# Kernel tuning notes

Measured on AMD Instinct MI355X. Metric: run time of the kernel, lower is better.

Reference implementation:

```python
import jax, jax.numpy as jnp
import numpy as np

B, N, C, H = 64, 500, 128, 256
EPS = 1e-5


def _bn(x, g, b):
    # BatchNorm1d in training mode: biased batch statistics
    m = jnp.mean(x, axis=0)
    v = jnp.mean((x - m) ** 2, axis=0)
    return g * (x - m) * jax.lax.rsqrt(v + EPS) + b


def _lin(x, w, b):
    return x @ w.T + b


def setup_inputs() -> dict:
    key = jax.random.key(0)
    ks = jax.random.split(key, 16)

    def w(k, shape, s=0.05):
        return (s * jax.random.normal(k, shape)).astype(jnp.float32)

    return {
        'l2_xyz': jax.random.uniform(ks[0], (B, 3, N), dtype=jnp.float32),
        'l2_points': jax.random.normal(ks[1], (B, C, N), dtype=jnp.float32),
        'l3_points': jax.random.normal(ks[2], (B, C), dtype=jnp.float32),
        'temp': jax.random.uniform(ks[3], (B, 1, N), dtype=jnp.float32) * 400.0,
        'fc_res0_w': w(ks[4], (H, H)), 'fc_res0_b': jnp.zeros((H,), jnp.float32),
        'bn_res0_g': jnp.ones((H,), jnp.float32), 'bn_res0_b': jnp.zeros((H,), jnp.float32),
        'fc_res1_w': w(ks[5], (H, H)), 'fc_res1_b': jnp.zeros((H,), jnp.float32),
        'bn_res1_g': jnp.ones((H,), jnp.float32), 'bn_res1_b': jnp.zeros((H,), jnp.float32),
        'fc_res2_w': w(ks[6], (H, H)), 'fc_res2_b': jnp.zeros((H,), jnp.float32),
        'bn_res2_g': jnp.ones((H,), jnp.float32), 'bn_res2_b': jnp.zeros((H,), jnp.float32),
        'fc_lt1_w': w(ks[7], (H, H)), 'fc_lt1_b': jnp.zeros((H,), jnp.float32),
        'bn_lt1_g': jnp.ones((H,), jnp.float32), 'bn_lt1_b': jnp.zeros((H,), jnp.float32),
        'fc_lt4_w': w(ks[8], (1, H)), 'fc_lt4_b': jnp.zeros((1,), jnp.float32),
    }


def reference(l2_xyz, l2_points, l3_points, temp,
              fc_res0_w, fc_res0_b, bn_res0_g, bn_res0_b,
              fc_res1_w, fc_res1_b, bn_res1_g, bn_res1_b,
              fc_res2_w, fc_res2_b, bn_res2_g, bn_res2_b,
              fc_lt1_w, fc_lt1_b, bn_lt1_g, bn_lt1_b,
              fc_lt4_w, fc_lt4_b):
    point = jnp.transpose(l2_xyz, (0, 2, 1))    # [B,N,3]
    data = jnp.transpose(l2_points, (0, 2, 1))  # [B,N,C]

    # square_distance(point, point), then abs + sqrt
    s = jnp.sum(point * point, axis=-1)  # [B,N]
    sq = s[:, :, None] + s[:, None, :] - 2.0 * jnp.einsum('bik,bjk->bij', point, point)
    dist = jnp.sqrt(jnp.abs(sq))  # [B,N,N]

    # distance-band edge set as a mask (torch.where -> variable edge list)
    mask = ((dist > 0.19) & (dist < 0.21)).astype(data.dtype)  # [B,N,N]
    counts = jnp.maximum(jnp.sum(mask, axis=(1, 2)), 1.0)      # [B] edges per batch

    # per-channel average of data[b,i,c]*data[b,j,c] over edges (b,i,j).
    # Identical math to the torch take/index_add channel loop over corr_matrix,
    # without materializing the [B,C,N,N] outer-product tensor.
    t = jnp.einsum('bij,bjc->bic', mask, data)                  # [B,N,C]
    correlation = jnp.einsum('bic,bic->bc', t, data) / counts[:, None]  # [B,C]

    sa4 = l3_points.reshape(B, C)
    c = jnp.concatenate([correlation, sa4], axis=1)  # [B,256]

    h = jax.nn.relu(_bn(_lin(c, fc_res0_w, fc_res0_b), bn_res0_g, bn_res0_b))
    h = jax.nn.relu(_bn(_lin(h, fc_res1_w, fc_res1_b), bn_res1_g, bn_res1_b))
    h = jax.nn.relu(_bn(_lin(h, fc_res2_w, fc_res2_b), bn_res2_g, bn_res2_b))
    h = jax.nn.relu(_bn(_lin(h, fc_lt1_w, fc_lt1_b), bn_lt1_g, bn_lt1_b))
    tc = _lin(h, fc_lt4_w, fc_lt4_b).squeeze(-1)  # [B]

    tsys = jnp.mean(temp, axis=2).squeeze(-1)     # [B]
    return (tc, tsys, l2_points, correlation)
```

## Files before the change

kernel.cpp:

```cpp
#include <hip/hip_runtime.h>

#define NB 64
#define NP 500
#define NC 128
#define NH 256
#define EPS_BN 1e-5f

#define SEGS 8
#define CAPE 1024

#define EDGE_OFF 0
#define EDGE_WORDS (NB * SEGS * CAPE)
#define CNT_OFF (EDGE_OFF + EDGE_WORDS)
#define CT_OFF (CNT_OFF + 512)
#define H1_OFF (CT_OFF + NH * NB)
#define H2_OFF (H1_OFF + NH * NB)

#define OUT_PTS_OFF 128
#define OUT_CORR_OFF 4096128

#define COPY_BLKS 768
#define TOTAL_F4 1024000

__global__ __launch_bounds__(256) void k1_scan_misc_copy(
    const float* __restrict__ xyz,
    const float* __restrict__ temp,
    const float* __restrict__ l3,
    const float* __restrict__ b4,
    const float* __restrict__ pts,
    float* __restrict__ out,
    float* __restrict__ ws) {
  const int blk = blockIdx.x;
  const int tid = threadIdx.x;

  if (blk < 512) {
    const int b = blk >> 3;
    const int jt = blk & 7;
    __shared__ float4 pt[NP];
    __shared__ int lcnt;
    if (tid == 0) lcnt = 0;
    const float* xr = xyz + b * 1500;
    for (int idx = tid; idx < NP; idx += 256) {
      float x = xr[idx], y = xr[500 + idx], z = xr[1000 + idx];
      float s = x * x + y * y + z * z;
      pt[idx] = make_float4(x, y, z, s);
    }
    __syncthreads();

    const int j0 = jt * 63;
    const int j1 = (j0 + 63 < NP) ? j0 + 63 : NP;
    const int i0 = tid;
    const int i1 = tid + 256;
    float4 p0 = pt[i0];
    float4 p1 = (i1 < NP) ? pt[i1] : make_float4(0.f, 0.f, 0.f, 0.f);
    int* eseg = (int*)ws + EDGE_OFF + (b * SEGS + jt) * CAPE;

    for (int j = j0; j < j1; ++j) {
      float4 q = pt[j];
      if (i0 < j) {
        float dot = p0.x * q.x + p0.y * q.y + p0.z * q.z;
        float sq = p0.w + q.w - 2.f * dot;
        float d = sqrtf(fabsf(sq));
        if (d > 0.19f && d < 0.21f) {
          int e = atomicAdd(&lcnt, 1);
          if (e < CAPE) eseg[e] = (i0 << 16) | j;
        }
      }
      if (i1 < j) {
        float dot = p1.x * q.x + p1.y * q.y + p1.z * q.z;
        float sq = p1.w + q.w - 2.f * dot;
        float d = sqrtf(fabsf(sq));
        if (d > 0.19f && d < 0.21f) {
          int e = atomicAdd(&lcnt, 1);
          if (e < CAPE) eseg[e] = (i1 << 16) | j;
        }
      }
    }
    __syncthreads();
    if (tid == 0) {
      int c = lcnt < CAPE ? lcnt : CAPE;
      ((int*)ws)[CNT_OFF + b * SEGS + jt] = c;
    }
  } else if (blk < 576) {
    const int b = blk - 512;
    float sum = 0.f;
    for (int i = tid; i < NP; i += 256) sum += temp[b * NP + i];
    for (int off = 32; off; off >>= 1) sum += __shfl_xor(sum, off);
    __shared__ float wsum[4];
    if ((tid & 63) == 0) wsum[tid >> 6] = sum;
    __syncthreads();
    if (tid == 0)
      out[64 + b] = (wsum[0] + wsum[1] + wsum[2] + wsum[3]) * (1.f / 500.f);
    if (tid < 128) ws[CT_OFF + (128 + tid) * 64 + b] = l3[b * NC + tid];
    if (tid == 0) out[b] = b4[0];
  } else {
    const int cb = blk - 576;
    const float4* src = (const float4*)pts;
    float4* dst = (float4*)(out + OUT_PTS_OFF);
    for (int idx = cb * 256 + tid; idx < TOTAL_F4 / 2; idx += COPY_BLKS * 256)
      dst[idx] = src[idx];
  }
}

__global__ __launch_bounds__(256) void k2_corr_copy(
    const float* __restrict__ data,
    float* __restrict__ out,
    float* __restrict__ ws) {
  const int blk = blockIdx.x;
  const int tid = threadIdx.x;

  if (blk < 512) {
    const int b = blk >> 3;
    const int c0 = (blk & 7) * 16;
    __shared__ float dT[NP * 20];
    __shared__ float corrp[16];
    if (tid < 16) corrp[tid] = 0.f;

    const float4* in4 = (const float4*)(data + (size_t)b * 64000 + c0 * 500);
    for (int idx = tid; idx < 2000; idx += 256) {
      float4 v = in4[idx];
      int c = idx / 125;
      int j = (idx - c * 125) * 4;
      dT[(j + 0) * 20 + c] = v.x;
      dT[(j + 1) * 20 + c] = v.y;
      dT[(j + 2) * 20 + c] = v.z;
      dT[(j + 3) * 20 + c] = v.w;
    }
    __syncthreads();

    const int quad = tid & 3;
    const int slot = tid >> 2;
    float4 acc = make_float4(0.f, 0.f, 0.f, 0.f);
    const int* cnts = (const int*)ws + CNT_OFF + b * SEGS;
    int Etot = 0;
    for (int seg = 0; seg < SEGS; ++seg) {
      int E = cnts[seg];
      Etot += E;
      const int* eseg = (const int*)ws + EDGE_OFF + (b * SEGS + seg) * CAPE;
      for (int e = slot; e < E; e += 64) {
        int ij = eseg[e];
        int i = ij >> 16, j = ij & 0xffff;
        const float4 a = *(const float4*)(dT + i * 20 + quad * 4);
        const float4 c4 = *(const float4*)(dT + j * 20 + quad * 4);
        acc.x += a.x * c4.x;
        acc.y += a.y * c4.y;
        acc.z += a.z * c4.z;
        acc.w += a.w * c4.w;
      }
    }
    for (int off = 4; off < 64; off <<= 1) {
      acc.x += __shfl_xor(acc.x, off);
      acc.y += __shfl_xor(acc.y, off);
      acc.z += __shfl_xor(acc.z, off);
      acc.w += __shfl_xor(acc.w, off);
    }
    if ((tid & 63) < 4) {
      atomicAdd(&corrp[quad * 4 + 0], acc.x);
      atomicAdd(&corrp[quad * 4 + 1], acc.y);
      atomicAdd(&corrp[quad * 4 + 2], acc.z);
      atomicAdd(&corrp[quad * 4 + 3], acc.w);
    }
    __syncthreads();
    if (tid < 16) {
      float denom = fmaxf(2.f * (float)Etot, 1.f);
      float v = 2.f * corrp[tid] / denom;
      out[OUT_CORR_OFF + b * NC + c0 + tid] = v;
      ws[CT_OFF + (c0 + tid) * 64 + b] = v;
    }
  } else {
    const int cb = blk - 512;
    const float4* src = (const float4*)data;
    float4* dst = (float4*)(out + OUT_PTS_OFF);
    for (int idx = TOTAL_F4 / 2 + cb * 256 + tid; idx < TOTAL_F4;
         idx += COPY_BLKS * 256)
      dst[idx] = src[idx];
  }
}

__global__ __launch_bounds__(256) void layer_k(
    const float* __restrict__ xT, const float* __restrict__ W,
    const float* __restrict__ bias, const float* __restrict__ g,
    const float* __restrict__ be, float* __restrict__ yT,
    const float* __restrict__ w4, float* __restrict__ tc) {
  const int o = blockIdx.x;
  const int b = threadIdx.x & 63;
  const int w = threadIdx.x >> 6;
  const float* wr = W + o * NH + w * 64;
  const float* xp = xT + (w * 64) * 64 + b;
  float acc = 0.f;
#pragma unroll
  for (int i = 0; i < 64; ++i) acc += xp[i * 64] * wr[i];
  __shared__ float part[4][64];
  part[w][b] = acc;
  __syncthreads();
  if (w == 0) {
    float t = part[0][b] + part[1][b] + part[2][b] + part[3][b] + bias[o];
    float s1 = t;
    for (int off = 32; off; off >>= 1) s1 += __shfl_xor(s1, off);
    float m = s1 * (1.f / 64.f);
    float d = t - m;
    float s2 = d * d;
    for (int off = 32; off; off >>= 1) s2 += __shfl_xor(s2, off);
    float var = s2 * (1.f / 64.f);
    float h = g[o] * d * rsqrtf(var + EPS_BN) + be[o];
    h = fmaxf(h, 0.f);
    if (w4) {
      atomicAdd(&tc[b], w4[o] * h);
    } else {
      yT[o * 64 + b] = h;
    }
  }
}

extern "C" void kernel_launch(void* const* d_in, const int* in_sizes, int n_in,
                              void* d_out, int out_size, void* d_ws,
                              size_t ws_size, hipStream_t stream) {
  const float* xyz = (const float*)d_in[0];
  const float* pts = (const float*)d_in[1];
  const float* l3 = (const float*)d_in[2];
  const float* temp = (const float*)d_in[3];
  const float* w0 = (const float*)d_in[4];
  const float* b0 = (const float*)d_in[5];
  const float* g0 = (const float*)d_in[6];
  const float* be0 = (const float*)d_in[7];
  const float* w1 = (const float*)d_in[8];
  const float* b1 = (const float*)d_in[9];
  const float* g1 = (const float*)d_in[10];
  const float* be1 = (const float*)d_in[11];
  const float* w2 = (const float*)d_in[12];
  const float* b2 = (const float*)d_in[13];
  const float* g2 = (const float*)d_in[14];
  const float* be2 = (const float*)d_in[15];
  const float* w3 = (const float*)d_in[16];
  const float* b3 = (const float*)d_in[17];
  const float* g3 = (const float*)d_in[18];
  const float* be3 = (const float*)d_in[19];
  const float* w4 = (const float*)d_in[20];
  const float* b4 = (const float*)d_in[21];

  float* out = (float*)d_out;
  float* ws = (float*)d_ws;
  float* cT = ws + CT_OFF;
  float* hA = ws + H1_OFF;
  float* hB = ws + H2_OFF;

  k1_scan_misc_copy<<<576 + COPY_BLKS, 256, 0, stream>>>(xyz, temp, l3, b4,
                                                         pts, out, ws);
  k2_corr_copy<<<512 + COPY_BLKS, 256, 0, stream>>>(pts, out, ws);
  layer_k<<<256, 256, 0, stream>>>(cT, w0, b0, g0, be0, hA, nullptr, nullptr);
  layer_k<<<256, 256, 0, stream>>>(hA, w1, b1, g1, be1, hB, nullptr, nullptr);
  layer_k<<<256, 256, 0, stream>>>(hB, w2, b2, g2, be2, hA, nullptr, nullptr);
  layer_k<<<256, 256, 0, stream>>>(hA, w3, b3, g3, be3, nullptr, w4, out);
}
```

Before: 165.2 us.

## Fuse edge scan and correlation into one kernel, dropping the edge list

Merges the distance-band scan and the per-channel correlation into a single kernel. Each block now owns one batch and a 16-channel slice, scans all point pairs itself, and accumulates the channel products directly in registers, so no edge list is written to or read back from global memory. Each block repeats the full pair scan once per channel slice, so distance work grows eightfold. There is one fewer kernel launch and the copy of the point data is handled in a single pass. The price is divergent inner loops with 16 register accumulators and larger shared memory per block, which may reduce occupancy.

Result: slower. 260.6 us (+57.7%).

```diff
diff --git a/kernel.cpp b/kernel.cpp
--- a/kernel.cpp
+++ b/kernel.cpp
@@ -6,117 +6,45 @@
 #define NH 256
 #define EPS_BN 1e-5f
 
-#define SEGS 8
-#define CAPE 1024
-
-#define EDGE_OFF 0
-#define EDGE_WORDS (NB * SEGS * CAPE)
-#define CNT_OFF (EDGE_OFF + EDGE_WORDS)
-#define CT_OFF (CNT_OFF + 512)
+#define CT_OFF 0
 #define H1_OFF (CT_OFF + NH * NB)
 #define H2_OFF (H1_OFF + NH * NB)
 
 #define OUT_PTS_OFF 128
 #define OUT_CORR_OFF 4096128
-
-#define COPY_BLKS 768
 #define TOTAL_F4 1024000
 
-__global__ __launch_bounds__(256) void k1_scan_misc_copy(
+#define SCAN_BLKS 512
+#define MISC_END 576
+#define KA_GRID 1600
+#define CPY_BLKS (KA_GRID - MISC_END)
+
+__global__ __launch_bounds__(256) void kA(
     const float* __restrict__ xyz,
+    const float* __restrict__ pts,
+    const float* __restrict__ l3,
     const float* __restrict__ temp,
-    const float* __restrict__ l3,
     const float* __restrict__ b4,
-    const float* __restrict__ pts,
     float* __restrict__ out,
     float* __restrict__ ws) {
   const int blk = blockIdx.x;
   const int tid = threadIdx.x;
 
-  if (blk < 512) {
+  __shared__ __align__(16) float smem[NP * 20 + 68];
+  __shared__ __align__(16) float4 pt[NP];
+
+  if (blk < SCAN_BLKS) {
     const int b = blk >> 3;
-    const int jt = blk & 7;
-    __shared__ float4 pt[NP];
-    __shared__ int lcnt;
-    if (tid == 0) lcnt = 0;
+    const int c0 = (blk & 7) * 16;
+    float* dT = smem;
+    float* partials = smem + NP * 20;
+
     const float* xr = xyz + b * 1500;
     for (int idx = tid; idx < NP; idx += 256) {
       float x = xr[idx], y = xr[500 + idx], z = xr[1000 + idx];
-      float s = x * x + y * y + z * z;
-      pt[idx] = make_float4(x, y, z, s);
-    }
-    __syncthreads();
-
-    const int j0 = jt * 63;
-    const int j1 = (j0 + 63 < NP) ? j0 + 63 : NP;
-    const int i0 = tid;
-    const int i1 = tid + 256;
-    float4 p0 = pt[i0];
-    float4 p1 = (i1 < NP) ? pt[i1] : make_float4(0.f, 0.f, 0.f, 0.f);
-    int* eseg = (int*)ws + EDGE_OFF + (b * SEGS + jt) * CAPE;
-
-    for (int j = j0; j < j1; ++j) {
-      float4 q = pt[j];
-      if (i0 < j) {
-        float dot = p0.x * q.x + p0.y * q.y + p0.z * q.z;
-        float sq = p0.w + q.w - 2.f * dot;
-        float d = sqrtf(fabsf(sq));
-        if (d > 0.19f && d < 0.21f) {
-          int e = atomicAdd(&lcnt, 1);
-          if (e < CAPE) eseg[e] = (i0 << 16) | j;
-        }
-      }
-      if (i1 < j) {
-        float dot = p1.x * q.x + p1.y * q.y + p1.z * q.z;
-        float sq = p1.w + q.w - 2.f * dot;
-        float d = sqrtf(fabsf(sq));
-        if (d > 0.19f && d < 0.21f) {
-          int e = atomicAdd(&lcnt, 1);
-          if (e < CAPE) eseg[e] = (i1 << 16) | j;
-        }
-      }
-    }
-    __syncthreads();
-    if (tid == 0) {
-      int c = lcnt < CAPE ? lcnt : CAPE;
-      ((int*)ws)[CNT_OFF + b * SEGS + jt] = c;
-    }
-  } else if (blk < 576) {
-    const int b = blk - 512;
-    float sum = 0.f;
-    for (int i = tid; i < NP; i += 256) sum += temp[b * NP + i];
-    for (int off = 32; off; off >>= 1) sum += __shfl_xor(sum, off);
-    __shared__ float wsum[4];
-    if ((tid & 63) == 0) wsum[tid >> 6] = sum;
-    __syncthreads();
-    if (tid == 0)
-      out[64 + b] = (wsum[0] + wsum[1] + wsum[2] + wsum[3]) * (1.f / 500.f);
-    if (tid < 128) ws[CT_OFF + (128 + tid) * 64 + b] = l3[b * NC + tid];
-    if (tid == 0) out[b] = b4[0];
-  } else {
-    const int cb = blk - 576;
-    const float4* src = (const float4*)pts;
-    float4* dst = (float4*)(out + OUT_PTS_OFF);
-    for (int idx = cb * 256 + tid; idx < TOTAL_F4 / 2; idx += COPY_BLKS * 256)
-      dst[idx] = src[idx];
-  }
-}
-
-__global__ __launch_bounds__(256) void k2_corr_copy(
-    const float* __restrict__ data,
-    float* __restrict__ out,
-    float* __restrict__ ws) {
-  const int blk = blockIdx.x;
-  const int tid = threadIdx.x;
-
-  if (blk < 512) {
-    const int b = blk >> 3;
-    const int c0 = (blk & 7) * 16;
-    __shared__ float dT[NP * 20];
-    __shared__ float corrp[16];
-    if (tid < 16) corrp[tid] = 0.f;
-
-    const float4* in4 = (const float4*)(data + (size_t)b * 64000 + c0 * 500);
+      pt[idx] = make_float4(x, y, z, x * x + y * y + z * z);
+    }
+    const float4* in4 = (const float4*)(pts + (size_t)b * 64000 + c0 * 500);
     for (int idx = tid; idx < 2000; idx += 256) {
       float4 v = in4[idx];
       int c = idx / 125;
@@ -128,51 +56,94 @@
     }
     __syncthreads();
 
-    const int quad = tid & 3;
-    const int slot = tid >> 2;
-    float4 acc = make_float4(0.f, 0.f, 0.f, 0.f);
-    const int* cnts = (const int*)ws + CNT_OFF + b * SEGS;
-    int Etot = 0;
-    for (int seg = 0; seg < SEGS; ++seg) {
-      int E = cnts[seg];
-      Etot += E;
-      const int* eseg = (const int*)ws + EDGE_OFF + (b * SEGS + seg) * CAPE;
-      for (int e = slot; e < E; e += 64) {
-        int ij = eseg[e];
-        int i = ij >> 16, j = ij & 0xffff;
-        const float4 a = *(const float4*)(dT + i * 20 + quad * 4);
-        const float4 c4 = *(const float4*)(dT + j * 20 + quad * 4);
-        acc.x += a.x * c4.x;
-        acc.y += a.y * c4.y;
-        acc.z += a.z * c4.z;
-        acc.w += a.w * c4.w;
+    const int i0 = tid;
+    const int i1 = tid + 256;
+    float4 p0 = pt[i0];
+    float4 p1 = (i1 < NP) ? pt[i1] : make_float4(0.f, 0.f, 0.f, 0.f);
+
+    float acc[16];
+#pragma unroll
+    for (int c = 0; c < 16; ++c) acc[c] = 0.f;
+    int ecnt = 0;
+
+    for (int j = 1; j < NP; ++j) {
+      float4 q = pt[j];
+      if (i0 < j) {
+        float dot = p0.x * q.x + p0.y * q.y + p0.z * q.z;
+        float sq = p0.w + q.w - 2.f * dot;
+        float d = sqrtf(fabsf(sq));
+        if (d > 0.19f && d < 0.21f) {
+          ++ecnt;
+          const float4* ai = (const float4*)(dT + i0 * 20);
+          const float4* aj = (const float4*)(dT + j * 20);
+#pragma unroll
+          for (int qd = 0; qd < 4; ++qd) {
+            float4 a = ai[qd], bb = aj[qd];
+            acc[4 * qd + 0] += a.x * bb.x;
+            acc[4 * qd + 1] += a.y * bb.y;
+            acc[4 * qd + 2] += a.z * bb.z;
+            acc[4 * qd + 3] += a.w * bb.w;
+          }
+        }
       }
-    }
-    for (int off = 4; off < 64; off <<= 1) {
-      acc.x += __shfl_xor(acc.x, off);
-      acc.y += __shfl_xor(acc.y, off);
-      acc.z += __shfl_xor(acc.z, off);
-      acc.w += __shfl_xor(acc.w, off);
-    }
-    if ((tid & 63) < 4) {
-      atomicAdd(&corrp[quad * 4 + 0], acc.x);
-      atomicAdd(&corrp[quad * 4 + 1], acc.y);
-      atomicAdd(&corrp[quad * 4 + 2], acc.z);
-      atomicAdd(&corrp[quad * 4 + 3], acc.w);
+      if (i1 < j) {
+        float dot = p1.x * q.x + p1.y * q.y + p1.z * q.z;
+        float sq = p1.w + q.w - 2.f * dot;
+        float d = sqrtf(fabsf(sq));
+        if (d > 0.19f && d < 0.21f) {
+          ++ecnt;
+          const float4* ai = (const float4*)(dT + i1 * 20);
+          const float4* aj = (const float4*)(dT + j * 20);
+#pragma unroll
+          for (int qd = 0; qd < 4; ++qd) {
+            float4 a = ai[qd], bb = aj[qd];
+            acc[4 * qd + 0] += a.x * bb.x;
+            acc[4 * qd + 1] += a.y * bb.y;
+            acc[4 * qd + 2] += a.z * bb.z;
+            acc[4 * qd + 3] += a.w * bb.w;
+          }
+        }
+      }
+    }
+
+#pragma unroll
+    for (int c = 0; c < 16; ++c)
+      for (int off = 32; off; off >>= 1) acc[c] += __shfl_xor(acc[c], off);
+    float ec = (float)ecnt;
+    for (int off = 32; off; off >>= 1) ec += __shfl_xor(ec, off);
+
+    const int w = tid >> 6;
+    if ((tid & 63) == 0) {
+#pragma unroll
+      for (int c = 0; c < 16; ++c) partials[w * 17 + c] = acc[c];
+      partials[w * 17 + 16] = ec;
     }
     __syncthreads();
     if (tid < 16) {
-      float denom = fmaxf(2.f * (float)Etot, 1.f);
-      float v = 2.f * corrp[tid] / denom;
+      float S = partials[tid] + partials[17 + tid] + partials[34 + tid] +
+                partials[51 + tid];
+      float E = partials[16] + partials[33] + partials[50] + partials[67];
+      float v = 2.f * S / fmaxf(2.f * E, 1.f);
       out[OUT_CORR_OFF + b * NC + c0 + tid] = v;
       ws[CT_OFF + (c0 + tid) * 64 + b] = v;
     }
+  } else if (blk < MISC_END) {
+    const int b = blk - SCAN_BLKS;
+    float sum = 0.f;
+    for (int i = tid; i < NP; i += 256) sum += temp[b * NP + i];
+    for (int off = 32; off; off >>= 1) sum += __shfl_xor(sum, off);
+    float* wsum = smem;
+    if ((tid & 63) == 0) wsum[tid >> 6] = sum;
+    __syncthreads();
+    if (tid == 0)
+      out[64 + b] = (wsum[0] + wsum[1] + wsum[2] + wsum[3]) * (1.f / 500.f);
+    if (tid < NC) ws[CT_OFF + (NC + tid) * 64 + b] = l3[b * NC + tid];
+    if (tid == 0) out[b] = b4[0];
   } else {
-    const int cb = blk - 512;
-    const float4* src = (const float4*)data;
+    const int cb = blk - MISC_END;
+    const float4* src = (const float4*)pts;
     float4* dst = (float4*)(out + OUT_PTS_OFF);
-    for (int idx = TOTAL_F4 / 2 + cb * 256 + tid; idx < TOTAL_F4;
-         idx += COPY_BLKS * 256)
+    for (int idx = cb * 256 + tid; idx < TOTAL_F4; idx += CPY_BLKS * 256)
       dst[idx] = src[idx];
   }
 }
@@ -244,9 +215,7 @@
   float* hA = ws + H1_OFF;
   float* hB = ws + H2_OFF;
 
-  k1_scan_misc_copy<<<576 + COPY_BLKS, 256, 0, stream>>>(xyz, temp, l3, b4,
-                                                         pts, out, ws);
-  k2_corr_copy<<<512 + COPY_BLKS, 256, 0, stream>>>(pts, out, ws);
+  kA<<<KA_GRID, 256, 0, stream>>>(xyz, pts, l3, temp, b4, out, ws);
   layer_k<<<256, 256, 0, stream>>>(cT, w0, b0, g0, be0, hA, nullptr, nullptr);
   layer_k<<<256, 256, 0, stream>>>(hA, w1, b1, g1, be1, hB, nullptr, nullptr);
   layer_k<<<256, 256, 0, stream>>>(hB, w2, b2, g2, be2, hA, nullptr, nullptr);
```

## Fuse all stages into one persistent kernel with global atomic flag synchronization

Applied to the files above, without the earlier changes.

Replaces six kernel launches with a single kernel in which scan, correlation, misc, copy and four MLP layers run as block roles coordinated through global atomic counters and spin-wait barriers. The edge scan and correlation for each batch now run in the same blocks, which wait for all eight segment blocks of their batch before consuming edges. The aim is to remove launch gaps and inter-kernel drain between small stages. The cost is a memset per call and reliance on all 1344 blocks being co-resident, since spinning blocks could otherwise deadlock.

After: 430.5 us. 2.61x slower.

```diff
diff --git a/kernel.cpp b/kernel.cpp
--- a/kernel.cpp
+++ b/kernel.cpp
@@ -10,191 +10,49 @@
 #define CAPE 1024
 
 #define EDGE_OFF 0
-#define EDGE_WORDS (NB * SEGS * CAPE)
-#define CNT_OFF (EDGE_OFF + EDGE_WORDS)
-#define CT_OFF (CNT_OFF + 512)
+#define CNT_OFF (NB * SEGS * CAPE)
+#define SYNC_OFF (CNT_OFF + 512)
+#define CT_OFF (SYNC_OFF + 128)
 #define H1_OFF (CT_OFF + NH * NB)
 #define H2_OFF (H1_OFF + NH * NB)
 
+#define SD_CORR 64
+#define SD_MISC 65
+#define SD_BAR 66
+
 #define OUT_PTS_OFF 128
 #define OUT_CORR_OFF 4096128
-
-#define COPY_BLKS 768
 #define TOTAL_F4 1024000
 
-__global__ __launch_bounds__(256) void k1_scan_misc_copy(
-    const float* __restrict__ xyz,
-    const float* __restrict__ temp,
-    const float* __restrict__ l3,
-    const float* __restrict__ b4,
-    const float* __restrict__ pts,
-    float* __restrict__ out,
-    float* __restrict__ ws) {
-  const int blk = blockIdx.x;
-  const int tid = threadIdx.x;
-
-  if (blk < 512) {
-    const int b = blk >> 3;
-    const int jt = blk & 7;
-    __shared__ float4 pt[NP];
-    __shared__ int lcnt;
-    if (tid == 0) lcnt = 0;
-    const float* xr = xyz + b * 1500;
-    for (int idx = tid; idx < NP; idx += 256) {
-      float x = xr[idx], y = xr[500 + idx], z = xr[1000 + idx];
-      float s = x * x + y * y + z * z;
-      pt[idx] = make_float4(x, y, z, s);
-    }
-    __syncthreads();
-
-    const int j0 = jt * 63;
-    const int j1 = (j0 + 63 < NP) ? j0 + 63 : NP;
-    const int i0 = tid;
-    const int i1 = tid + 256;
-    float4 p0 = pt[i0];
-    float4 p1 = (i1 < NP) ? pt[i1] : make_float4(0.f, 0.f, 0.f, 0.f);
-    int* eseg = (int*)ws + EDGE_OFF + (b * SEGS + jt) * CAPE;
-
-    for (int j = j0; j < j1; ++j) {
-      float4 q = pt[j];
-      if (i0 < j) {
-        float dot = p0.x * q.x + p0.y * q.y + p0.z * q.z;
-        float sq = p0.w + q.w - 2.f * dot;
-        float d = sqrtf(fabsf(sq));
-        if (d > 0.19f && d < 0.21f) {
-          int e = atomicAdd(&lcnt, 1);
-          if (e < CAPE) eseg[e] = (i0 << 16) | j;
-        }
-      }
-      if (i1 < j) {
-        float dot = p1.x * q.x + p1.y * q.y + p1.z * q.z;
-        float sq = p1.w + q.w - 2.f * dot;
-        float d = sqrtf(fabsf(sq));
-        if (d > 0.19f && d < 0.21f) {
-          int e = atomicAdd(&lcnt, 1);
-          if (e < CAPE) eseg[e] = (i1 << 16) | j;
-        }
-      }
-    }
-    __syncthreads();
-    if (tid == 0) {
-      int c = lcnt < CAPE ? lcnt : CAPE;
-      ((int*)ws)[CNT_OFF + b * SEGS + jt] = c;
-    }
-  } else if (blk < 576) {
-    const int b = blk - 512;
-    float sum = 0.f;
-    for (int i = tid; i < NP; i += 256) sum += temp[b * NP + i];
-    for (int off = 32; off; off >>= 1) sum += __shfl_xor(sum, off);
-    __shared__ float wsum[4];
-    if ((tid & 63) == 0) wsum[tid >> 6] = sum;
-    __syncthreads();
-    if (tid == 0)
-      out[64 + b] = (wsum[0] + wsum[1] + wsum[2] + wsum[3]) * (1.f / 500.f);
-    if (tid < 128) ws[CT_OFF + (128 + tid) * 64 + b] = l3[b * NC + tid];
-    if (tid == 0) out[b] = b4[0];
-  } else {
-    const int cb = blk - 576;
-    const float4* src = (const float4*)pts;
-    float4* dst = (float4*)(out + OUT_PTS_OFF);
-    for (int idx = cb * 256 + tid; idx < TOTAL_F4 / 2; idx += COPY_BLKS * 256)
-      dst[idx] = src[idx];
-  }
-}
-
-__global__ __launch_bounds__(256) void k2_corr_copy(
-    const float* __restrict__ data,
-    float* __restrict__ out,
-    float* __restrict__ ws) {
-  const int blk = blockIdx.x;
-  const int tid = threadIdx.x;
-
-  if (blk < 512) {
-    const int b = blk >> 3;
-    const int c0 = (blk & 7) * 16;
-    __shared__ float dT[NP * 20];
-    __shared__ float corrp[16];
-    if (tid < 16) corrp[tid] = 0.f;
-
-    const float4* in4 = (const float4*)(data + (size_t)b * 64000 + c0 * 500);
-    for (int idx = tid; idx < 2000; idx += 256) {
-      float4 v = in4[idx];
-      int c = idx / 125;
-      int j = (idx - c * 125) * 4;
-      dT[(j + 0) * 20 + c] = v.x;
-      dT[(j + 1) * 20 + c] = v.y;
-      dT[(j + 2) * 20 + c] = v.z;
-      dT[(j + 3) * 20 + c] = v.w;
-    }
-    __syncthreads();
-
-    const int quad = tid & 3;
-    const int slot = tid >> 2;
-    float4 acc = make_float4(0.f, 0.f, 0.f, 0.f);
-    const int* cnts = (const int*)ws + CNT_OFF + b * SEGS;
-    int Etot = 0;
-    for (int seg = 0; seg < SEGS; ++seg) {
-      int E = cnts[seg];
-      Etot += E;
-      const int* eseg = (const int*)ws + EDGE_OFF + (b * SEGS + seg) * CAPE;
-      for (int e = slot; e < E; e += 64) {
-        int ij = eseg[e];
-        int i = ij >> 16, j = ij & 0xffff;
-        const float4 a = *(const float4*)(dT + i * 20 + quad * 4);
-        const float4 c4 = *(const float4*)(dT + j * 20 + quad * 4);
-        acc.x += a.x * c4.x;
-        acc.y += a.y * c4.y;
-        acc.z += a.z * c4.z;
-        acc.w += a.w * c4.w;
-      }
-    }
-    for (int off = 4; off < 64; off <<= 1) {
-      acc.x += __shfl_xor(acc.x, off);
-      acc.y += __shfl_xor(acc.y, off);
-      acc.z += __shfl_xor(acc.z, off);
-      acc.w += __shfl_xor(acc.w, off);
-    }
-    if ((tid & 63) < 4) {
-      atomicAdd(&corrp[quad * 4 + 0], acc.x);
-      atomicAdd(&corrp[quad * 4 + 1], acc.y);
-      atomicAdd(&corrp[quad * 4 + 2], acc.z);
-      atomicAdd(&corrp[quad * 4 + 3], acc.w);
-    }
-    __syncthreads();
-    if (tid < 16) {
-      float denom = fmaxf(2.f * (float)Etot, 1.f);
-      float v = 2.f * corrp[tid] / denom;
-      out[OUT_CORR_OFF + b * NC + c0 + tid] = v;
-      ws[CT_OFF + (c0 + tid) * 64 + b] = v;
-    }
-  } else {
-    const int cb = blk - 512;
-    const float4* src = (const float4*)data;
-    float4* dst = (float4*)(out + OUT_PTS_OFF);
-    for (int idx = TOTAL_F4 / 2 + cb * 256 + tid; idx < TOTAL_F4;
-         idx += COPY_BLKS * 256)
-      dst[idx] = src[idx];
-  }
-}
-
-__global__ __launch_bounds__(256) void layer_k(
-    const float* __restrict__ xT, const float* __restrict__ W,
-    const float* __restrict__ bias, const float* __restrict__ g,
-    const float* __restrict__ be, float* __restrict__ yT,
-    const float* __restrict__ w4, float* __restrict__ tc) {
-  const int o = blockIdx.x;
-  const int b = threadIdx.x & 63;
-  const int w = threadIdx.x >> 6;
+#define CORR_BLKS 512
+#define MISC_END 576
+#define COPY_BLKS 512
+#define COPY_END (MISC_END + COPY_BLKS)
+#define GRID_TOT (COPY_END + NH)
+
+__device__ __forceinline__ int ldacq(const int* p) {
+  return __hip_atomic_load(p, __ATOMIC_ACQUIRE, __HIP_MEMORY_SCOPE_AGENT);
+}
+__device__ __forceinline__ void addrel(int* p, int v) {
+  __hip_atomic_fetch_add(p, v, __ATOMIC_RELEASE, __HIP_MEMORY_SCOPE_AGENT);
+}
+
+__device__ __forceinline__ void mlp_layer(int o, int tid, const float* xT,
+                                          const float* W, const float* bias,
+                                          const float* g, const float* be,
+                                          float* yT, const float* w4,
+                                          float* tc, float* part) {
+  const int b = tid & 63;
+  const int w = tid >> 6;
   const float* wr = W + o * NH + w * 64;
   const float* xp = xT + (w * 64) * 64 + b;
   float acc = 0.f;
 #pragma unroll
   for (int i = 0; i < 64; ++i) acc += xp[i * 64] * wr[i];
-  __shared__ float part[4][64];
-  part[w][b] = acc;
+  part[w * 64 + b] = acc;
   __syncthreads();
   if (w == 0) {
-    float t = part[0][b] + part[1][b] + part[2][b] + part[3][b] + bias[o];
+    float t = part[b] + part[64 + b] + part[128 + b] + part[192 + b] + bias[o];
     float s1 = t;
     for (int off = 32; off; off >>= 1) s1 += __shfl_xor(s1, off);
     float m = s1 * (1.f / 64.f);
@@ -209,6 +67,192 @@
     } else {
       yT[o * 64 + b] = h;
     }
+  }
+  __syncthreads();
+}
+
+__device__ __forceinline__ void mlp_bar(int* ctr) {
+  __threadfence();
+  __syncthreads();
+  if (threadIdx.x == 0) {
+    addrel(ctr, 1);
+    while (ldacq(ctr) < NH) __builtin_amdgcn_s_sleep(8);
+  }
+  __syncthreads();
+}
+
+__global__ __launch_bounds__(256) void mega(
+    const float* __restrict__ xyz,
+    const float* __restrict__ pts,
+    const float* __restrict__ l3,
+    const float* __restrict__ temp,
+    const float* __restrict__ w0, const float* __restrict__ b0,
+    const float* __restrict__ g0, const float* __restrict__ be0,
+    const float* __restrict__ w1, const float* __restrict__ b1,
+    const float* __restrict__ g1, const float* __restrict__ be1,
+    const float* __restrict__ w2, const float* __restrict__ b2,
+    const float* __restrict__ g2, const float* __restrict__ be2,
+    const float* __restrict__ w3, const float* __restrict__ b3,
+    const float* __restrict__ g3, const float* __restrict__ be3,
+    const float* __restrict__ w4, const float* __restrict__ b4,
+    float* __restrict__ out, float* __restrict__ ws) {
+  const int blk = blockIdx.x;
+  const int tid = threadIdx.x;
+
+  __shared__ __align__(16) float smem[NP * 20 + 68];
+  __shared__ int lcnt;
+  int* syncw = (int*)ws + SYNC_OFF;
+
+  if (blk < CORR_BLKS) {
+    const int b = blk >> 3;
+    const int g = blk & 7;
+    const int c0 = g * 16;
+    float* dT = smem;
+    float* corrp = smem + NP * 20;
+
+    float4* pt = (float4*)smem;
+    if (tid == 0) lcnt = 0;
+    if (tid < 16) corrp[tid] = 0.f;
+    const float* xr = xyz + b * 1500;
+    for (int idx = tid; idx < NP; idx += 256) {
+      float x = xr[idx], y = xr[500 + idx], z = xr[1000 + idx];
+      pt[idx] = make_float4(x, y, z, x * x + y * y + z * z);
+    }
+    __syncthreads();
+
+    const int j0 = g * 63;
+    const int j1 = (j0 + 63 < NP) ? j0 + 63 : NP;
+    const int i0 = tid;
+    const int i1 = tid + 256;
+    float4 p0 = pt[i0];
+    float4 p1 = (i1 < NP) ? pt[i1] : make_float4(0.f, 0.f, 0.f, 0.f);
+    int* eseg = (int*)ws + EDGE_OFF + (b * SEGS + g) * CAPE;
+
+    for (int j = j0; j < j1; ++j) {
+      float4 q = pt[j];
+      if (i0 < j) {
+        float sq = p0.w + q.w - 2.f * (p0.x * q.x + p0.y * q.y + p0.z * q.z);
+        float d = sqrtf(fabsf(sq));
+        if (d > 0.19f && d < 0.21f) {
+          int e = atomicAdd(&lcnt, 1);
+          if (e < CAPE) eseg[e] = (i0 << 16) | j;
+        }
+      }
+      if (i1 < j) {
+        float sq = p1.w + q.w - 2.f * (p1.x * q.x + p1.y * q.y + p1.z * q.z);
+        float d = sqrtf(fabsf(sq));
+        if (d > 0.19f && d < 0.21f) {
+          int e = atomicAdd(&lcnt, 1);
+          if (e < CAPE) eseg[e] = (i1 << 16) | j;
+        }
+      }
+    }
+    __threadfence();
+    __syncthreads();
+    if (tid == 0) {
+      int c = lcnt < CAPE ? lcnt : CAPE;
+      ((int*)ws)[CNT_OFF + b * SEGS + g] = c;
+      __threadfence();
+      addrel(&syncw[b], 1);
+    }
+
+    const float4* in4 = (const float4*)(pts + (size_t)b * 64000 + c0 * 500);
+    for (int idx = tid; idx < 2000; idx += 256) {
+      float4 v = in4[idx];
+      int c = idx / 125;
+      int j = (idx - c * 125) * 4;
+      dT[(j + 0) * 20 + c] = v.x;
+      dT[(j + 1) * 20 + c] = v.y;
+      dT[(j + 2) * 20 + c] = v.z;
+      dT[(j + 3) * 20 + c] = v.w;
+    }
+    if (tid == 0)
+      while (ldacq(&syncw[b]) < SEGS) __builtin_amdgcn_s_sleep(4);
+    __syncthreads();
+
+    const int quad = tid & 3;
+    const int slot = tid >> 2;
+    float4 acc = make_float4(0.f, 0.f, 0.f, 0.f);
+    const int* cnts = (const int*)ws + CNT_OFF + b * SEGS;
+    int Etot = 0;
+    for (int seg = 0; seg < SEGS; ++seg) {
+      int E = cnts[seg];
+      Etot += E;
+      const int* es = (const int*)ws + EDGE_OFF + (b * SEGS + seg) * CAPE;
+      for (int e = slot; e < E; e += 64) {
+        int ij = es[e];
+        int i = ij >> 16, j = ij & 0xffff;
+        const float4 a = *(const float4*)(dT + i * 20 + quad * 4);
+        const float4 c4 = *(const float4*)(dT + j * 20 + quad * 4);
+        acc.x += a.x * c4.x;
+        acc.y += a.y * c4.y;
+        acc.z += a.z * c4.z;
+        acc.w += a.w * c4.w;
+      }
+    }
+    for (int off = 4; off < 64; off <<= 1) {
+      acc.x += __shfl_xor(acc.x, off);
+      acc.y += __shfl_xor(acc.y, off);
+      acc.z += __shfl_xor(acc.z, off);
+      acc.w += __shfl_xor(acc.w, off);
+    }
+    if ((tid & 63) < 4) {
+      atomicAdd(&corrp[quad * 4 + 0], acc.x);
+      atomicAdd(&corrp[quad * 4 + 1], acc.y);
+      atomicAdd(&corrp[quad * 4 + 2], acc.z);
+      atomicAdd(&corrp[quad * 4 + 3], acc.w);
+    }
+    __syncthreads();
+    if (tid < 16) {
+      float denom = fmaxf(2.f * (float)Etot, 1.f);
+      float v = 2.f * corrp[tid] / denom;
+      out[OUT_CORR_OFF + b * NC + c0 + tid] = v;
+      ws[CT_OFF + (c0 + tid) * 64 + b] = v;
+    }
+    __threadfence();
+    __syncthreads();
+    if (tid == 0) addrel(&syncw[SD_CORR], 1);
+  } else if (blk < MISC_END) {
+    const int b = blk - CORR_BLKS;
+    float sum = 0.f;
+    for (int i = tid; i < NP; i += 256) sum += temp[b * NP + i];
+    for (int off = 32; off; off >>= 1) sum += __shfl_xor(sum, off);
+    float* wsum = smem;
+    if ((tid & 63) == 0) wsum[tid >> 6] = sum;
+    __syncthreads();
+    if (tid == 0)
+      out[64 + b] = (wsum[0] + wsum[1] + wsum[2] + wsum[3]) * (1.f / 500.f);
+    if (tid < NC) ws[CT_OFF + (NC + tid) * 64 + b] = l3[b * NC + tid];
+    if (tid == 0) out[b] = b4[0];
+    __threadfence();
+    __syncthreads();
+    if (tid == 0) addrel(&syncw[SD_MISC], 1);
+  } else if (blk < COPY_END) {
+    const int cb = blk - MISC_END;
+    const float4* src = (const float4*)pts;
+    float4* dst = (float4*)(out + OUT_PTS_OFF);
+    for (int idx = cb * 256 + tid; idx < TOTAL_F4; idx += COPY_BLKS * 256)
+      dst[idx] = src[idx];
+  } else {
+    const int o = blk - COPY_END;
+    float* cT = ws + CT_OFF;
+    float* hA = ws + H1_OFF;
+    float* hB = ws + H2_OFF;
+    float* part = smem;
+
+    if (tid == 0)
+      while (ldacq(&syncw[SD_CORR]) < CORR_BLKS ||
+             ldacq(&syncw[SD_MISC]) < NB)
+        __builtin_amdgcn_s_sleep(16);
+    __syncthreads();
+
+    mlp_layer(o, tid, cT, w0, b0, g0, be0, hA, nullptr, nullptr, part);
+    mlp_bar(&syncw[SD_BAR + 0]);
+    mlp_layer(o, tid, hA, w1, b1, g1, be1, hB, nullptr, nullptr, part);
+    mlp_bar(&syncw[SD_BAR + 1]);
+    mlp_layer(o, tid, hB, w2, b2, g2, be2, hA, nullptr, nullptr, part);
+    mlp_bar(&syncw[SD_BAR + 2]);
+    mlp_layer(o, tid, hA, w3, b3, g3, be3, nullptr, w4, out, part);
   }
 }
 
@@ -240,15 +284,10 @@
 
   float* out = (float*)d_out;
   float* ws = (float*)d_ws;
-  float* cT = ws + CT_OFF;
-  float* hA = ws + H1_OFF;
-  float* hB = ws + H2_OFF;
-
-  k1_scan_misc_copy<<<576 + COPY_BLKS, 256, 0, stream>>>(xyz, temp, l3, b4,
-                                                         pts, out, ws);
-  k2_corr_copy<<<512 + COPY_BLKS, 256, 0, stream>>>(pts, out, ws);
-  layer_k<<<256, 256, 0, stream>>>(cT, w0, b0, g0, be0, hA, nullptr, nullptr);
-  layer_k<<<256, 256, 0, stream>>>(hA, w1, b1, g1, be1, hB, nullptr, nullptr);
-  layer_k<<<256, 256, 0, stream>>>(hB, w2, b2, g2, be2, hA, nullptr, nullptr);
-  layer_k<<<256, 256, 0, stream>>>(hA, w3, b3, g3, be3, nullptr, w4, out);
-}
+
+  hipMemsetAsync((char*)d_ws + SYNC_OFF * sizeof(float), 0,
+                 128 * sizeof(float), stream);
+  mega<<<GRID_TOT, 256, 0, stream>>>(xyz, pts, l3, temp, w0, b0, g0, be0, w1,
+                                     b1, g1, be1, w2, b2, g2, be2, w3, b3, g3,
+                                     be3, w4, b4, out, ws);
+}
```

## Fuse four MLP layers into one single-block MFMA kernel with split-bf16 GEMM

Applied to the files above, without the earlier changes.

Replaces the four per-layer launches with a single one-block kernel. It keeps the 256x64 activation in LDS and computes each layer with bf16 MFMA using a hi/lo split (three MFMAs per tile) to stay close to fp32 accuracy, with batchnorm and ReLU applied in registers. It drops the linear bias because batch-stat BN cancels it, and moves the whole points copy into k1 so k2 only does correlation. The trade is three launches and global round-trips removed in exchange for a serial one-workgroup GEMM chain that uses only one CU.

Measured after the change: 199.4 us. +20.7%, slower.

```diff
diff --git a/kernel.cpp b/kernel.cpp
--- a/kernel.cpp
+++ b/kernel.cpp
@@ -10,30 +10,39 @@
 #define CAPE 1024
 
 #define EDGE_OFF 0
-#define EDGE_WORDS (NB * SEGS * CAPE)
-#define CNT_OFF (EDGE_OFF + EDGE_WORDS)
+#define CNT_OFF (NB * SEGS * CAPE)
 #define CT_OFF (CNT_OFF + 512)
-#define H1_OFF (CT_OFF + NH * NB)
-#define H2_OFF (H1_OFF + NH * NB)
 
 #define OUT_PTS_OFF 128
 #define OUT_CORR_OFF 4096128
-
-#define COPY_BLKS 768
 #define TOTAL_F4 1024000
+
+#define SCAN_BLKS 512
+#define MISC_END 576
+#define K1_COPY 1024
+#define K1_GRID (MISC_END + K1_COPY)
+
+typedef __attribute__((ext_vector_type(8))) short short8b;
+typedef __attribute__((ext_vector_type(4))) float f32x4;
+
+__device__ __forceinline__ short bfh(float f) {
+  return (short)(__builtin_bit_cast(unsigned, f) >> 16);
+}
+__device__ __forceinline__ float bff(short h) {
+  return __builtin_bit_cast(float, ((unsigned)(unsigned short)h) << 16);
+}
 
 __global__ __launch_bounds__(256) void k1_scan_misc_copy(
     const float* __restrict__ xyz,
     const float* __restrict__ temp,
     const float* __restrict__ l3,
-    const float* __restrict__ b4,
     const float* __restrict__ pts,
     float* __restrict__ out,
     float* __restrict__ ws) {
   const int blk = blockIdx.x;
   const int tid = threadIdx.x;
 
-  if (blk < 512) {
+  if (blk < SCAN_BLKS) {
     const int b = blk >> 3;
     const int jt = blk & 7;
     __shared__ float4 pt[NP];
@@ -42,8 +51,7 @@
     const float* xr = xyz + b * 1500;
     for (int idx = tid; idx < NP; idx += 256) {
       float x = xr[idx], y = xr[500 + idx], z = xr[1000 + idx];
-      float s = x * x + y * y + z * z;
-      pt[idx] = make_float4(x, y, z, s);
+      pt[idx] = make_float4(x, y, z, x * x + y * y + z * z);
     }
     __syncthreads();
 
@@ -58,8 +66,7 @@
     for (int j = j0; j < j1; ++j) {
       float4 q = pt[j];
       if (i0 < j) {
-        float dot = p0.x * q.x + p0.y * q.y + p0.z * q.z;
-        float sq = p0.w + q.w - 2.f * dot;
+        float sq = p0.w + q.w - 2.f * (p0.x * q.x + p0.y * q.y + p0.z * q.z);
         float d = sqrtf(fabsf(sq));
         if (d > 0.19f && d < 0.21f) {
           int e = atomicAdd(&lcnt, 1);
@@ -67,8 +74,7 @@
         }
       }
       if (i1 < j) {
-        float dot = p1.x * q.x + p1.y * q.y + p1.z * q.z;
-        float sq = p1.w + q.w - 2.f * dot;
+        float sq = p1.w + q.w - 2.f * (p1.x * q.x + p1.y * q.y + p1.z * q.z);
         float d = sqrtf(fabsf(sq));
         if (d > 0.19f && d < 0.21f) {
           int e = atomicAdd(&lcnt, 1);
@@ -81,8 +87,8 @@
       int c = lcnt < CAPE ? lcnt : CAPE;
       ((int*)ws)[CNT_OFF + b * SEGS + jt] = c;
     }
-  } else if (blk < 576) {
-    const int b = blk - 512;
+  } else if (blk < MISC_END) {
+    const int b = blk - SCAN_BLKS;
     float sum = 0.f;
     for (int i = tid; i < NP; i += 256) sum += temp[b * NP + i];
     for (int off = 32; off; off >>= 1) sum += __shfl_xor(sum, off);
@@ -91,123 +97,233 @@
     __syncthreads();
     if (tid == 0)
       out[64 + b] = (wsum[0] + wsum[1] + wsum[2] + wsum[3]) * (1.f / 500.f);
-    if (tid < 128) ws[CT_OFF + (128 + tid) * 64 + b] = l3[b * NC + tid];
-    if (tid == 0) out[b] = b4[0];
+    if (tid < NC) ws[CT_OFF + (NC + tid) * 64 + b] = l3[b * NC + tid];
   } else {
-    const int cb = blk - 576;
+    const int cb = blk - MISC_END;
     const float4* src = (const float4*)pts;
     float4* dst = (float4*)(out + OUT_PTS_OFF);
-    for (int idx = cb * 256 + tid; idx < TOTAL_F4 / 2; idx += COPY_BLKS * 256)
+    for (int idx = cb * 256 + tid; idx < TOTAL_F4; idx += K1_COPY * 256)
       dst[idx] = src[idx];
   }
 }
 
-__global__ __launch_bounds__(256) void k2_corr_copy(
+__global__ __launch_bounds__(256) void k2_corr(
     const float* __restrict__ data,
     float* __restrict__ out,
     float* __restrict__ ws) {
   const int blk = blockIdx.x;
   const int tid = threadIdx.x;
-
-  if (blk < 512) {
-    const int b = blk >> 3;
-    const int c0 = (blk & 7) * 16;
-    __shared__ float dT[NP * 20];
-    __shared__ float corrp[16];
-    if (tid < 16) corrp[tid] = 0.f;
-
-    const float4* in4 = (const float4*)(data + (size_t)b * 64000 + c0 * 500);
-    for (int idx = tid; idx < 2000; idx += 256) {
-      float4 v = in4[idx];
-      int c = idx / 125;
-      int j = (idx - c * 125) * 4;
-      dT[(j + 0) * 20 + c] = v.x;
-      dT[(j + 1) * 20 + c] = v.y;
-      dT[(j + 2) * 20 + c] = v.z;
-      dT[(j + 3) * 20 + c] = v.w;
-    }
+  const int b = blk >> 3;
+  const int c0 = (blk & 7) * 16;
+  __shared__ float dT[NP * 20];
+  __shared__ float corrp[16];
+  if (tid < 16) corrp[tid] = 0.f;
+
+  const float4* in4 = (const float4*)(data + (size_t)b * 64000 + c0 * 500);
+  for (int idx = tid; idx < 2000; idx += 256) {
+    float4 v = in4[idx];
+    int c = idx / 125;
+    int j = (idx - c * 125) * 4;
+    dT[(j + 0) * 20 + c] = v.x;
+    dT[(j + 1) * 20 + c] = v.y;
+    dT[(j + 2) * 20 + c] = v.z;
+    dT[(j + 3) * 20 + c] = v.w;
+  }
+  __syncthreads();
+
+  const int quad = tid & 3;
+  const int slot = tid >> 2;
+  float4 acc = make_float4(0.f, 0.f, 0.f, 0.f);
+  const int* cnts = (const int*)ws + CNT_OFF + b * SEGS;
+  int Etot = 0;
+  for (int seg = 0; seg < SEGS; ++seg) {
+    int E = cnts[seg];
+    Etot += E;
+    const int* eseg = (const int*)ws + EDGE_OFF + (b * SEGS + seg) * CAPE;
+    for (int e = slot; e < E; e += 64) {
+      int ij = eseg[e];
+      int i = ij >> 16, j = ij & 0xffff;
+      const float4 a = *(const float4*)(dT + i * 20 + quad * 4);
+      const float4 c4 = *(const float4*)(dT + j * 20 + quad * 4);
+      acc.x += a.x * c4.x;
+      acc.y += a.y * c4.y;
+      acc.z += a.z * c4.z;
+      acc.w += a.w * c4.w;
+    }
+  }
+  for (int off = 4; off < 64; off <<= 1) {
+    acc.x += __shfl_xor(acc.x, off);
+    acc.y += __shfl_xor(acc.y, off);
+    acc.z += __shfl_xor(acc.z, off);
+    acc.w += __shfl_xor(acc.w, off);
+  }
+  if ((tid & 63) < 4) {
+    atomicAdd(&corrp[quad * 4 + 0], acc.x);
+    atomicAdd(&corrp[quad * 4 + 1], acc.y);
+    atomicAdd(&corrp[quad * 4 + 2], acc.z);
+    atomicAdd(&corrp[quad * 4 + 3], acc.w);
+  }
+  __syncthreads();
+  if (tid < 16) {
+    float denom = fmaxf(2.f * (float)Etot, 1.f);
+    float v = 2.f * corrp[tid] / denom;
+    out[OUT_CORR_OFF + b * NC + c0 + tid] = v;
+    ws[CT_OFF + (c0 + tid) * 64 + b] = v;
+  }
+}
+
+__device__ __forceinline__ void gemm_layer(const float* xT, const float* W,
+                                           f32x4 (&acc)[4][4], int wv,
+                                           int l15, int lg) {
+#pragma unroll
+  for (int t = 0; t < 4; ++t)
+#pragma unroll
+    for (int n = 0; n < 4; ++n) acc[t][n] = (f32x4){0.f, 0.f, 0.f, 0.f};
+
+  for (int s = 0; s < 8; ++s) {
+    short8b bh[4], bl[4];
+#pragma unroll
+    for (int n = 0; n < 4; ++n) {
+#pragma unroll
+      for (int i = 0; i < 8; ++i) {
+        float f = xT[(s * 32 + lg * 8 + i) * 64 + n * 16 + l15];
+        short h = bfh(f);
+        bh[n][i] = h;
+        bl[n][i] = bfh(f - bff(h));
+      }
+    }
+#pragma unroll
+    for (int t = 0; t < 4; ++t) {
+      const float* wr = W + (wv * 64 + t * 16 + l15) * 256 + s * 32 + lg * 8;
+      float4 wa = *(const float4*)wr;
+      float4 wb = *(const float4*)(wr + 4);
+      short8b ah, al;
+#pragma unroll
+      for (int i = 0; i < 4; ++i) {
+        float fa = ((const float*)&wa)[i];
+        short ha = bfh(fa);
+        ah[i] = ha;
+        al[i] = bfh(fa - bff(ha));
+        float fb = ((const float*)&wb)[i];
+        short hb = bfh(fb);
+        ah[4 + i] = hb;
+        al[4 + i] = bfh(fb - bff(hb));
+      }
+#pragma unroll
+      for (int n = 0; n < 4; ++n) {
+        acc[t][n] = __builtin_amdgcn_mfma_f32_16x16x32_bf16(ah, bh[n],
+                                                            acc[t][n], 0, 0, 0);
+        acc[t][n] = __builtin_amdgcn_mfma_f32_16x16x32_bf16(ah, bl[n],
+                                                            acc[t][n], 0, 0, 0);
+        acc[t][n] = __builtin_amdgcn_mfma_f32_16x16x32_bf16(al, bh[n],
+                                                            acc[t][n], 0, 0, 0);
+      }
+    }
+  }
+}
+
+__global__ __launch_bounds__(256) void k3_mlp(
+    const float* __restrict__ ws, const float* __restrict__ w0,
+    const float* __restrict__ g0, const float* __restrict__ be0,
+    const float* __restrict__ w1, const float* __restrict__ g1,
+    const float* __restrict__ be1, const float* __restrict__ w2,
+    const float* __restrict__ g2, const float* __restrict__ be2,
+    const float* __restrict__ w3, const float* __restrict__ g3,
+    const float* __restrict__ be3, const float* __restrict__ w4,
+    const float* __restrict__ b4, float* __restrict__ out) {
+  const int tid = threadIdx.x;
+  const int lane = tid & 63;
+  const int wv = tid >> 6;
+  const int l15 = lane & 15;
+  const int lg = lane >> 4;
+
+  __shared__ __align__(16) float xT[NH * NB];
+  __shared__ float tcl[NB];
+
+  const float4* src = (const float4*)(ws + CT_OFF);
+  float4* dst4 = (float4*)xT;
+  for (int i = tid; i < NH * NB / 4; i += 256) dst4[i] = src[i];
+  if (tid < NB) tcl[tid] = 0.f;
+  __syncthreads();
+
+  f32x4 acc[4][4];
+  const float* Ws[4] = {w0, w1, w2, w3};
+  const float* Gs[4] = {g0, g1, g2, g3};
+  const float* Bs[4] = {be0, be1, be2, be3};
+
+#pragma unroll
+  for (int L = 0; L < 4; ++L) {
+    gemm_layer(xT, Ws[L], acc, wv, l15, lg);
     __syncthreads();
 
-    const int quad = tid & 3;
-    const int slot = tid >> 2;
-    float4 acc = make_float4(0.f, 0.f, 0.f, 0.f);
-    const int* cnts = (const int*)ws + CNT_OFF + b * SEGS;
-    int Etot = 0;
-    for (int seg = 0; seg < SEGS; ++seg) {
-      int E = cnts[seg];
-      Etot += E;
-      const int* eseg = (const int*)ws + EDGE_OFF + (b * SEGS + seg) * CAPE;
-      for (int e = slot; e < E; e += 64) {
-        int ij = eseg[e];
-        int i = ij >> 16, j = ij & 0xffff;
-        const float4 a = *(const float4*)(dT + i * 20 + quad * 4);
-        const float4 c4 = *(const float4*)(dT + j * 20 + quad * 4);
-        acc.x += a.x * c4.x;
-        acc.y += a.y * c4.y;
-        acc.z += a.z * c4.z;
-        acc.w += a.w * c4.w;
-      }
-    }
-    for (int off = 4; off < 64; off <<= 1) {
-      acc.x += __shfl_xor(acc.x, off);
-      acc.y += __shfl_xor(acc.y, off);
-      acc.z += __shfl_xor(acc.z, off);
-      acc.w += __shfl_xor(acc.w, off);
-    }
-    if ((tid & 63) < 4) {
-      atomicAdd(&corrp[quad * 4 + 0], acc.x);
-      atomicAdd(&corrp[quad * 4 + 1], acc.y);
-      atomicAdd(&corrp[quad * 4 + 2], acc.z);
-      atomicAdd(&corrp[quad * 4 + 3], acc.w);
-    }
-    __syncthreads();
-    if (tid < 16) {
-      float denom = fmaxf(2.f * (float)Etot, 1.f);
-      float v = 2.f * corrp[tid] / denom;
-      out[OUT_CORR_OFF + b * NC + c0 + tid] = v;
-      ws[CT_OFF + (c0 + tid) * 64 + b] = v;
-    }
-  } else {
-    const int cb = blk - 512;
-    const float4* src = (const float4*)data;
-    float4* dst = (float4*)(out + OUT_PTS_OFF);
-    for (int idx = TOTAL_F4 / 2 + cb * 256 + tid; idx < TOTAL_F4;
-         idx += COPY_BLKS * 256)
-      dst[idx] = src[idx];
-  }
-}
-
-__global__ __launch_bounds__(256) void layer_k(
-    const float* __restrict__ xT, const float* __restrict__ W,
-    const float* __restrict__ bias, const float* __restrict__ g,
-    const float* __restrict__ be, float* __restrict__ yT,
-    const float* __restrict__ w4, float* __restrict__ tc) {
-  const int o = blockIdx.x;
-  const int b = threadIdx.x & 63;
-  const int w = threadIdx.x >> 6;
-  const float* wr = W + o * NH + w * 64;
-  const float* xp = xT + (w * 64) * 64 + b;
-  float acc = 0.f;
-#pragma unroll
-  for (int i = 0; i < 64; ++i) acc += xp[i * 64] * wr[i];
-  __shared__ float part[4][64];
-  part[w][b] = acc;
-  __syncthreads();
-  if (w == 0) {
-    float t = part[0][b] + part[1][b] + part[2][b] + part[3][b] + bias[o];
-    float s1 = t;
-    for (int off = 32; off; off >>= 1) s1 += __shfl_xor(s1, off);
-    float m = s1 * (1.f / 64.f);
-    float d = t - m;
-    float s2 = d * d;
-    for (int off = 32; off; off >>= 1) s2 += __shfl_xor(s2, off);
-    float var = s2 * (1.f / 64.f);
-    float h = g[o] * d * rsqrtf(var + EPS_BN) + be[o];
-    h = fmaxf(h, 0.f);
-    if (w4) {
-      atomicAdd(&tc[b], w4[o] * h);
+    if (L < 3) {
+#pragma unroll
+      for (int t = 0; t < 4; ++t) {
+#pragma unroll
+        for (int r = 0; r < 4; ++r) {
+          const int o = wv * 64 + t * 16 + lg * 4 + r;
+          float s1 = acc[t][0][r] + acc[t][1][r] + acc[t][2][r] + acc[t][3][r];
+          s1 += __shfl_xor(s1, 1);
+          s1 += __shfl_xor(s1, 2);
+          s1 += __shfl_xor(s1, 4);
+          s1 += __shfl_xor(s1, 8);
+          float m = s1 * (1.f / 64.f);
+          float d0 = acc[t][0][r] - m, d1 = acc[t][1][r] - m;
+          float d2 = acc[t][2][r] - m, d3 = acc[t][3][r] - m;
+          float s2 = d0 * d0 + d1 * d1 + d2 * d2 + d3 * d3;
+          s2 += __shfl_xor(s2, 1);
+          s2 += __shfl_xor(s2, 2);
+          s2 += __shfl_xor(s2, 4);
+          s2 += __shfl_xor(s2, 8);
+          float sc = Gs[L][o] * rsqrtf(s2 * (1.f / 64.f) + EPS_BN);
+          float bo = Bs[L][o];
+          xT[o * 64 + 0 * 16 + l15] = fmaxf(d0 * sc + bo, 0.f);
+          xT[o * 64 + 1 * 16 + l15] = fmaxf(d1 * sc + bo, 0.f);
+          xT[o * 64 + 2 * 16 + l15] = fmaxf(d2 * sc + bo, 0.f);
+          xT[o * 64 + 3 * 16 + l15] = fmaxf(d3 * sc + bo, 0.f);
+        }
+      }
+      __syncthreads();
     } else {
-      yT[o * 64 + b] = h;
+      float part[4] = {0.f, 0.f, 0.f, 0.f};
+#pragma unroll
+      for (int t = 0; t < 4; ++t) {
+#pragma unroll
+        for (int r = 0; r < 4; ++r) {
+          const int o = wv * 64 + t * 16 + lg * 4 + r;
+          float s1 = acc[t][0][r] + acc[t][1][r] + acc[t][2][r] + acc[t][3][r];
+          s1 += __shfl_xor(s1, 1);
+          s1 += __shfl_xor(s1, 2);
+          s1 += __shfl_xor(s1, 4);
+          s1 += __shfl_xor(s1, 8);
+          float m = s1 * (1.f / 64.f);
+          float d0 = acc[t][0][r] - m, d1 = acc[t][1][r] - m;
+          float d2 = acc[t][2][r] - m, d3 = acc[t][3][r] - m;
+          float s2 = d0 * d0 + d1 * d1 + d2 * d2 + d3 * d3;
+          s2 += __shfl_xor(s2, 1);
+          s2 += __shfl_xor(s2, 2);
+          s2 += __shfl_xor(s2, 4);
+          s2 += __shfl_xor(s2, 8);
+          float sc = Gs[3][o] * rsqrtf(s2 * (1.f / 64.f) + EPS_BN);
+          float bo = Bs[3][o];
+          float w4o = w4[o];
+          part[0] += fmaxf(d0 * sc + bo, 0.f) * w4o;
+          part[1] += fmaxf(d1 * sc + bo, 0.f) * w4o;
+          part[2] += fmaxf(d2 * sc + bo, 0.f) * w4o;
+          part[3] += fmaxf(d3 * sc + bo, 0.f) * w4o;
+        }
+      }
+#pragma unroll
+      for (int n = 0; n < 4; ++n) {
+        part[n] += __shfl_xor(part[n], 16);
+        part[n] += __shfl_xor(part[n], 32);
+      }
+      if (lg == 0) {
+#pragma unroll
+        for (int n = 0; n < 4; ++n) atomicAdd(&tcl[n * 16 + l15], part[n]);
+      }
+      __syncthreads();
+      if (tid < NB) out[tid] = b4[0] + tcl[tid];
     }
   }
 }
@@ -220,19 +336,15 @@
   const float* l3 = (const float*)d_in[2];
   const float* temp = (const float*)d_in[3];
   const float* w0 = (const float*)d_in[4];
-  const float* b0 = (const float*)d_in[5];
   const float* g0 = (const float*)d_in[6];
   const float* be0 = (const float*)d_in[7];
   const float* w1 = (const float*)d_in[8];
-  const float* b1 = (const float*)d_in[9];
   const float* g1 = (const float*)d_in[10];
   const float* be1 = (const float*)d_in[11];
   const float* w2 = (const float*)d_in[12];
-  const float* b2 = (const float*)d_in[13];
   const float* g2 = (const float*)d_in[14];
   const float* be2 = (const float*)d_in[15];
   const float* w3 = (const float*)d_in[16];
-  const float* b3 = (const float*)d_in[17];
   const float* g3 = (const float*)d_in[18];
   const float* be3 = (const float*)d_in[19];
   const float* w4 = (const float*)d_in[20];
@@ -240,15 +352,9 @@
 
   float* out = (float*)d_out;
   float* ws = (float*)d_ws;
-  float* cT = ws + CT_OFF;
-  float* hA = ws + H1_OFF;
-  float* hB = ws + H2_OFF;
-
-  k1_scan_misc_copy<<<576 + COPY_BLKS, 256, 0, stream>>>(xyz, temp, l3, b4,
-                                                         pts, out, ws);
-  k2_corr_copy<<<512 + COPY_BLKS, 256, 0, stream>>>(pts, out, ws);
-  layer_k<<<256, 256, 0, stream>>>(cT, w0, b0, g0, be0, hA, nullptr, nullptr);
-  layer_k<<<256, 256, 0, stream>>>(hA, w1, b1, g1, be1, hB, nullptr, nullptr);
-  layer_k<<<256, 256, 0, stream>>>(hB, w2, b2, g2, be2, hA, nullptr, nullptr);
-  layer_k<<<256, 256, 0, stream>>>(hA, w3, b3, g3, be3, nullptr, w4, out);
-}
+
+  k1_scan_misc_copy<<<K1_GRID, 256, 0, stream>>>(xyz, temp, l3, pts, out, ws);
+  k2_corr<<<512, 256, 0, stream>>>(pts, out, ws);
+  k3_mlp<<<1, 256, 0, stream>>>(ws, w0, g0, be0, w1, g1, be1, w2, g2, be2, w3,
+                                g3, be3, w4, b4, out);
+}
```
